# Performance work log

Measured on AMD Instinct MI355X. Metric: run time of the kernel, lower is better.

Reference implementation:

```python
import jax, jax.numpy as jnp
import numpy as np

N = 5
RANK = 3
IMW = IMH = 1024
S = IMW * IMH
RANKLIST = [1] + [RANK] * (N - 1) + [1]  # [1,3,3,3,3,1]


def _xavier_std(shape):
    # torch xavier_normal_ on a 3D tensor (a, b, c): fan_in = b*c, fan_out = a*c
    a, b, c = shape
    fan_in, fan_out = b * c, a * c
    return float(np.sqrt(2.0 / (fan_in + fan_out)))


def setup_inputs() -> dict:
    key = jax.random.key(0)
    keys = jax.random.split(key, N + 1)
    inp = {"z": jax.random.normal(keys[0], (S,), dtype=jnp.float32)}
    for n in range(N):
        shp = (RANKLIST[n], S, RANKLIST[n + 1])
        inp[f"TT{n}"] = jax.random.normal(keys[n + 1], shp, dtype=jnp.float32) * _xavier_std(shp)
    return inp


def reference(z, TT0, TT1, TT2, TT3, TT4):
    # V[k] = z @ TT[k] : contract the s axis -> (r_k, r_{k+1}); tiny matrices.
    f = jnp.einsum('s,rsq->rq', z, TT0)          # (1, 3)
    for core in (TT1, TT2, TT3):
        f = f @ jnp.einsum('s,rsq->rq', z, core)  # (1, 3)
    # Last factor: the slice TT[N-1][:, :, 0] itself (NOT contracted with z).
    f = f @ TT4[:, :, 0]                          # (1, s)
    return f.reshape(-1)                          # (s,)
```

## Files before the change

### kernel.cpp

```cpp
#include <hip/hip_runtime.h>

#define SDIM (1024 * 1024)
#define GROUPS (SDIM / 4)
#define GPT 2
#define CHUNKS (GROUPS / (256 * GPT))
#define NPLANE 10

__global__ __launch_bounds__(256) void ftt_k1(
    const float* __restrict__ z,
    const float* __restrict__ t0,
    const float* __restrict__ t1,
    const float* __restrict__ t2,
    const float* __restrict__ t3,
    float* __restrict__ partials)
{
    const int plane = blockIdx.y;

    const float* base;
    if (plane == 0) {
        base = t0;
    } else {
        const int pk = plane - 1;
        const int k = pk / 3;
        const float* tk = (k == 0) ? t1 : (k == 1) ? t2 : t3;
        base = tk + (pk % 3) * (3 * SDIM);
    }

    const int gA = blockIdx.x * (256 * GPT) + threadIdx.x;
    const int gB = gA + 256;

    const float4 zA = reinterpret_cast<const float4*>(z)[gA];
    const float4 zB = reinterpret_cast<const float4*>(z)[gB];
    const float4* pA = reinterpret_cast<const float4*>(base + 12 * gA);
    const float4* pB = reinterpret_cast<const float4*>(base + 12 * gB);
    const float4 a0 = pA[0], a1 = pA[1], a2 = pA[2];
    const float4 b0 = pB[0], b1 = pB[1], b2 = pB[2];

    float s0, s1, s2;
    s0  = zA.x * a0.x + zA.y * a0.w + zA.z * a1.z + zA.w * a2.y;
    s1  = zA.x * a0.y + zA.y * a1.x + zA.z * a1.w + zA.w * a2.z;
    s2  = zA.x * a0.z + zA.y * a1.y + zA.z * a2.x + zA.w * a2.w;
    s0 += zB.x * b0.x + zB.y * b0.w + zB.z * b1.z + zB.w * b2.y;
    s1 += zB.x * b0.y + zB.y * b1.x + zB.z * b1.w + zB.w * b2.z;
    s2 += zB.x * b0.z + zB.y * b1.y + zB.z * b2.x + zB.w * b2.w;

    #pragma unroll
    for (int off = 32; off > 0; off >>= 1) {
        s0 += __shfl_down(s0, off, 64);
        s1 += __shfl_down(s1, off, 64);
        s2 += __shfl_down(s2, off, 64);
    }

    __shared__ float red[4][3];
    const int lane = threadIdx.x & 63;
    const int wave = threadIdx.x >> 6;
    if (lane == 0) { red[wave][0] = s0; red[wave][1] = s1; red[wave][2] = s2; }
    __syncthreads();
    if (threadIdx.x < 3) {
        const int c = threadIdx.x;
        const float s = red[0][c] + red[1][c] + red[2][c] + red[3][c];
        partials[(plane * CHUNKS + blockIdx.x) * 4 + c] = s;
    }
}

__global__ __launch_bounds__(256) void ftt_k2(
    const float* __restrict__ partials,
    float* __restrict__ fvec)
{
    __shared__ float red[NPLANE * 3][8];
    const int job = threadIdx.x >> 3;
    const int sub = threadIdx.x & 7;
    if (job < NPLANE * 3) {
        const int plane = job / 3, c = job % 3;
        float s = 0.0f;
        const int b0 = sub * (CHUNKS / 8);
        #pragma unroll 4
        for (int b = b0; b < b0 + (CHUNKS / 8); ++b)
            s += partials[(plane * CHUNKS + b) * 4 + c];
        red[job][sub] = s;
    }
    __syncthreads();

    if (threadIdx.x == 0) {
        float sum[NPLANE * 3];
        #pragma unroll
        for (int i = 0; i < NPLANE * 3; ++i) {
            float t = 0.0f;
            #pragma unroll
            for (int g = 0; g < 8; ++g) t += red[i][g];
            sum[i] = t;
        }
        float f0 = sum[0], f1 = sum[1], f2 = sum[2];
        #pragma unroll
        for (int k = 0; k < 3; ++k) {
            const float* V = &sum[3 + k * 9];
            const float n0 = f0 * V[0] + f1 * V[3] + f2 * V[6];
            const float n1 = f0 * V[1] + f1 * V[4] + f2 * V[7];
            const float n2 = f0 * V[2] + f1 * V[5] + f2 * V[8];
            f0 = n0; f1 = n1; f2 = n2;
        }
        fvec[0] = f0; fvec[1] = f1; fvec[2] = f2;
    }
}

__global__ __launch_bounds__(256) void ftt_k3(
    const float* __restrict__ t4,
    const float* __restrict__ fvec,
    float* __restrict__ out)
{
    const int i0 = (blockIdx.x * blockDim.x + threadIdx.x) * 2;
    const float f0 = fvec[0], f1 = fvec[1], f2 = fvec[2];
    const float4* pa = reinterpret_cast<const float4*>(t4);
    const float4* pb = reinterpret_cast<const float4*>(t4 + SDIM);
    const float4* pc = reinterpret_cast<const float4*>(t4 + 2 * SDIM);
    const float4 aA = pa[i0], bA = pb[i0], cA = pc[i0];
    const float4 aB = pa[i0 + 1], bB = pb[i0 + 1], cB = pc[i0 + 1];
    float4 oA, oB;
    oA.x = f0 * aA.x + f1 * bA.x + f2 * cA.x;
    oA.y = f0 * aA.y + f1 * bA.y + f2 * cA.y;
    oA.z = f0 * aA.z + f1 * bA.z + f2 * cA.z;
    oA.w = f0 * aA.w + f1 * bA.w + f2 * cA.w;
    oB.x = f0 * aB.x + f1 * bB.x + f2 * cB.x;
    oB.y = f0 * aB.y + f1 * bB.y + f2 * cB.y;
    oB.z = f0 * aB.z + f1 * bB.z + f2 * cB.z;
    oB.w = f0 * aB.w + f1 * bB.w + f2 * cB.w;
    reinterpret_cast<float4*>(out)[i0] = oA;
    reinterpret_cast<float4*>(out)[i0 + 1] = oB;
}

extern "C" void kernel_launch(void* const* d_in, const int* in_sizes, int n_in,
                              void* d_out, int out_size, void* d_ws, size_t ws_size,
                              hipStream_t stream)
{
    const float* z  = (const float*)d_in[0];
    const float* t0 = (const float*)d_in[1];
    const float* t1 = (const float*)d_in[2];
    const float* t2 = (const float*)d_in[3];
    const float* t3 = (const float*)d_in[4];
    const float* t4 = (const float*)d_in[5];
    float* out = (float*)d_out;

    float* partials = (float*)d_ws;
    float* fvec     = partials + NPLANE * CHUNKS * 4;

    ftt_k1<<<dim3(CHUNKS, NPLANE), 256, 0, stream>>>(z, t0, t1, t2, t3, partials);
    ftt_k2<<<1, 256, 0, stream>>>(partials, fvec);
    ftt_k3<<<SDIM / 4 / 256 / 2, 256, 0, stream>>>(t4, fvec, out);
}
```

Baseline: 170.3 us.

## Coalesce TT core loads by lane-contiguous float4 reads with shared z tile

Reworks the plane-reduction kernel so that each wave reads the TT core slab as contiguous float4s across lanes, instead of each thread reading three strided float4s. z is staged in shared memory, and each lane picks the matching z entries and output column using its phase modulo 3. Output columns are rotated back before the wave reduction. The aim is better memory coalescing on the bandwidth-bound load, at the cost of extra index math, an added barrier and LDS traffic.

After: 173.9 us. +2.1%, slower.

```diff
diff --git a/kernel.cpp b/kernel.cpp
--- a/kernel.cpp
+++ b/kernel.cpp
@@ -1,9 +1,8 @@
 #include <hip/hip_runtime.h>
 
 #define SDIM (1024 * 1024)
-#define GROUPS (SDIM / 4)
-#define GPT 2
-#define CHUNKS (GROUPS / (256 * GPT))
+#define TILE_S 1024
+#define CHUNKS (SDIM / TILE_S)
 #define NPLANE 10
 
 __global__ __launch_bounds__(256) void ftt_k1(
@@ -15,51 +14,78 @@
     float* __restrict__ partials)
 {
     const int plane = blockIdx.y;
+    const int tile  = blockIdx.x;
+    const int tid   = threadIdx.x;
+    const int w     = tid >> 6;
+    const int lane  = tid & 63;
 
     const float* base;
     if (plane == 0) {
         base = t0;
     } else {
         const int pk = plane - 1;
-        const int k = pk / 3;
+        const int k  = pk / 3;
         const float* tk = (k == 0) ? t1 : (k == 1) ? t2 : t3;
         base = tk + (pk % 3) * (3 * SDIM);
     }
 
-    const int gA = blockIdx.x * (256 * GPT) + threadIdx.x;
-    const int gB = gA + 256;
+    __shared__ float zt[TILE_S];
+    const float4 z4 = reinterpret_cast<const float4*>(z)[tile * 256 + tid];
 
-    const float4 zA = reinterpret_cast<const float4*>(z)[gA];
-    const float4 zB = reinterpret_cast<const float4*>(z)[gB];
-    const float4* pA = reinterpret_cast<const float4*>(base + 12 * gA);
-    const float4* pB = reinterpret_cast<const float4*>(base + 12 * gB);
-    const float4 a0 = pA[0], a1 = pA[1], a2 = pA[2];
-    const float4 b0 = pB[0], b1 = pB[1], b2 = pB[2];
+    const float4* b4 = reinterpret_cast<const float4*>(base)
+                     + (size_t)tile * 768 + w * 192 + lane;
+    const float4 v0 = b4[0];
+    const float4 v1 = b4[64];
+    const float4 v2 = b4[128];
 
-    float s0, s1, s2;
-    s0  = zA.x * a0.x + zA.y * a0.w + zA.z * a1.z + zA.w * a2.y;
-    s1  = zA.x * a0.y + zA.y * a1.x + zA.z * a1.w + zA.w * a2.z;
-    s2  = zA.x * a0.z + zA.y * a1.y + zA.z * a2.x + zA.w * a2.w;
-    s0 += zB.x * b0.x + zB.y * b0.w + zB.z * b1.z + zB.w * b2.y;
-    s1 += zB.x * b0.y + zB.y * b1.x + zB.z * b1.w + zB.w * b2.z;
-    s2 += zB.x * b0.z + zB.y * b1.y + zB.z * b2.x + zB.w * b2.w;
+    reinterpret_cast<float4*>(zt)[tid] = z4;
+    __syncthreads();
+
+    float b0 = 0.f, b1 = 0.f, b2 = 0.f;
+    const int phi = lane % 3;
+
+    {
+        const int s0 = w * 256 + (4 * lane) / 3;
+        const float za = zt[s0], zb = zt[s0 + 1];
+        const int p = phi;
+        const float zm1 = (p < 2) ? za : zb;
+        const float zm2 = (p == 0) ? za : zb;
+        b0 += v0.x * za;  b1 += v0.y * zm1;  b2 += v0.z * zm2;  b0 += v0.w * zb;
+    }
+    {
+        const int s0 = w * 256 + (256 + 4 * lane) / 3;
+        const float za = zt[s0], zb = zt[s0 + 1];
+        int p = phi + 1; if (p >= 3) p -= 3;
+        const float zm1 = (p < 2) ? za : zb;
+        const float zm2 = (p == 0) ? za : zb;
+        b1 += v1.x * za;  b2 += v1.y * zm1;  b0 += v1.z * zm2;  b1 += v1.w * zb;
+    }
+    {
+        const int s0 = w * 256 + (512 + 4 * lane) / 3;
+        const float za = zt[s0], zb = zt[s0 + 1];
+        int p = phi + 2; if (p >= 3) p -= 3;
+        const float zm1 = (p < 2) ? za : zb;
+        const float zm2 = (p == 0) ? za : zb;
+        b2 += v2.x * za;  b0 += v2.y * zm1;  b1 += v2.z * zm2;  b2 += v2.w * zb;
+    }
+
+    float a0 = (phi == 0) ? b0 : (phi == 1) ? b2 : b1;
+    float a1 = (phi == 0) ? b1 : (phi == 1) ? b0 : b2;
+    float a2 = (phi == 0) ? b2 : (phi == 1) ? b1 : b0;
 
     #pragma unroll
     for (int off = 32; off > 0; off >>= 1) {
-        s0 += __shfl_down(s0, off, 64);
-        s1 += __shfl_down(s1, off, 64);
-        s2 += __shfl_down(s2, off, 64);
+        a0 += __shfl_down(a0, off, 64);
+        a1 += __shfl_down(a1, off, 64);
+        a2 += __shfl_down(a2, off, 64);
     }
 
     __shared__ float red[4][3];
-    const int lane = threadIdx.x & 63;
-    const int wave = threadIdx.x >> 6;
-    if (lane == 0) { red[wave][0] = s0; red[wave][1] = s1; red[wave][2] = s2; }
+    if (lane == 0) { red[w][0] = a0; red[w][1] = a1; red[w][2] = a2; }
     __syncthreads();
-    if (threadIdx.x < 3) {
-        const int c = threadIdx.x;
-        const float s = red[0][c] + red[1][c] + red[2][c] + red[3][c];
-        partials[(plane * CHUNKS + blockIdx.x) * 4 + c] = s;
+    if (tid < 3) {
+        const float s = red[0][tid] + red[1][tid] + red[2][tid] + red[3][tid];
+        partials[(plane * CHUNKS + tile) * 4 + tid] = s;
     }
 }
 
```
